# Kernel tuning notes

Measured on AMD Instinct MI355X. Metric: run time of the kernel, lower is better.

## Reference

```python
import jax, jax.numpy as jnp
import numpy as np

EMBED_DIM = 512
NUM_HEADS = 8
HEAD_DIM = EMBED_DIM // NUM_HEADS
SCALE = HEAD_DIM ** -0.5
B, N = 4, 2048


def setup_inputs() -> dict:
    key = jax.random.key(0)
    ks = jax.random.split(key, 6)
    x = jax.random.normal(ks[0], (B, N, EMBED_DIM), dtype=jnp.float32)
    mask = jnp.ones((B, N, N), dtype=jnp.int32)
    # nn.Linear params: weight [out, in], bias [out]
    lim_qkv = 1.0 / np.sqrt(EMBED_DIM)
    qkv_w = jax.random.uniform(ks[1], (3 * EMBED_DIM, EMBED_DIM), jnp.float32, -lim_qkv, lim_qkv)
    qkv_b = jax.random.uniform(ks[2], (3 * EMBED_DIM,), jnp.float32, -lim_qkv, lim_qkv)
    proj_w = jax.random.uniform(ks[3], (EMBED_DIM, EMBED_DIM), jnp.float32, -lim_qkv, lim_qkv)
    proj_b = jax.random.uniform(ks[4], (EMBED_DIM,), jnp.float32, -lim_qkv, lim_qkv)
    return {"x": x, "qkv_w": qkv_w, "qkv_b": qkv_b, "proj_w": proj_w, "proj_b": proj_b, "mask": mask}


def reference(x, qkv_w, qkv_b, proj_w, proj_b, mask):
    Bb, Nn, C = x.shape
    qkv = (jnp.einsum('bnc,oc->bno', x, qkv_w) + qkv_b).reshape(Bb, Nn, 3, NUM_HEADS, HEAD_DIM)
    qkv = jnp.transpose(qkv, (2, 0, 3, 1, 4))
    q, k, v = qkv[0], qkv[1], qkv[2]
    # full score matrix [B,H,N,N] (faithful to the unfused original)
    attn = jnp.einsum('bhnd,bhmd->bhnm', q, k) * SCALE
    attn = jnp.where(mask[:, None, :, :] == 0, -jnp.inf, attn)
    attn = jax.nn.softmax(attn, axis=-1)
    out = jnp.einsum('bhnm,bhmd->bhnd', attn, v)
    out = jnp.transpose(out, (0, 2, 1, 3)).reshape(Bb, Nn, C)
    out = jnp.einsum('bnc,oc->bno', out, proj_w) + proj_b
    return out
```

## Files before the change

### kernel.cpp

```cpp
#include <hip/hip_runtime.h>
#include <hip/hip_bf16.h>
#include <stdint.h>

#define NB 4
#define NH 8
#define SEQ 2048
#define HD 64
#define CDIM 512

using bf16 = __hip_bfloat16;
typedef __attribute__((ext_vector_type(8))) short short8;
typedef __attribute__((ext_vector_type(4))) short short4_t;
typedef __attribute__((ext_vector_type(2))) unsigned int uint2_t;
typedef __attribute__((ext_vector_type(4))) float f32x4;

#define NEG_BIG (-3.0e38f)
#define SOFT_C 0.18033688011112042f

__device__ __forceinline__ short bf16_bits(float x) {
  return __builtin_bit_cast(short, __float2bfloat16(x));
}

__device__ __forceinline__ void pack_p4(float a, float b, float c, float d, short* dst) {
  unsigned lo = (unsigned)(unsigned short)bf16_bits(a) |
                ((unsigned)(unsigned short)bf16_bits(b) << 16);
  unsigned hi = (unsigned)(unsigned short)bf16_bits(c) |
                ((unsigned)(unsigned short)bf16_bits(d) << 16);
  uint2_t t;
  t[0] = lo;
  t[1] = hi;
  *(uint2_t*)dst = t;
}

__device__ __forceinline__ void gld_lds16(const void* g, void* l) {
  __builtin_amdgcn_global_load_lds(
      (const __attribute__((address_space(1))) unsigned int*)g,
      (__attribute__((address_space(3))) unsigned int*)l, 16, 0, 0);
}

#define X4 1048576
#define Q4 196608
#define P4 65536
__global__ __launch_bounds__(256) void prep_cvt(const float* __restrict__ x,
                                                const float* __restrict__ wq,
                                                const float* __restrict__ wp,
                                                short* __restrict__ xb,
                                                short* __restrict__ wqb,
                                                short* __restrict__ wpb) {
  int idx = blockIdx.x * 256 + threadIdx.x;
  int stride = gridDim.x * 256;
  for (int i = idx; i < X4 + Q4 + P4; i += stride) {
    const float* src; short* dst; int off;
    if (i < X4)            { src = x;  dst = xb;  off = i; }
    else if (i < X4 + Q4)  { src = wq; dst = wqb; off = i - X4; }
    else                   { src = wp; dst = wpb; off = i - X4 - Q4; }
    f32x4 v = *(const f32x4*)(src + (size_t)off * 4);
    short4_t o;
    o[0] = bf16_bits(v[0]); o[1] = bf16_bits(v[1]);
    o[2] = bf16_bits(v[2]); o[3] = bf16_bits(v[3]);
    *(short4_t*)(dst + (size_t)off * 4) = o;
  }
}

__global__ __launch_bounds__(256) void qkv_union(const short* __restrict__ Xb,
                                                 const short* __restrict__ Wb,
                                                 const float* __restrict__ bias,
                                                 const int* __restrict__ mask,
                                                 unsigned long long* __restrict__ bits,
                                                 bf16* __restrict__ q,
                                                 bf16* __restrict__ k,
                                                 bf16* __restrict__ vt) {
  __shared__ short Alds[128][32];
  __shared__ short Blds[128][32];
  const int tid = threadIdx.x;
  const int lane = tid & 63;
  const int w = tid >> 6;

  if (blockIdx.x < 512) {
    int wave_g = blockIdx.x * 4 + w;
#pragma unroll 1
    for (int i = 0; i < 32; i++) {
      size_t c = (size_t)i * 2048 + wave_g;
      size_t base = c * 256;
      int v0 = mask[base + 0 * 64 + lane];
      int v1 = mask[base + 1 * 64 + lane];
      int v2 = mask[base + 2 * 64 + lane];
      int v3 = mask[base + 3 * 64 + lane];
      unsigned long long w0 = __ballot(v0 != 0);
      unsigned long long w1 = __ballot(v1 != 0);
      unsigned long long w2 = __ballot(v2 != 0);
      unsigned long long w3 = __ballot(v3 != 0);
      if (lane == 0) {
        bits[c * 4 + 0] = w0; bits[c * 4 + 1] = w1;
        bits[c * 4 + 2] = w2; bits[c * 4 + 3] = w3;
      }
    }
    return;
  }

  const int g = blockIdx.x - 512;
  const int wm = w >> 1, wn = w & 1;
  const int row0 = (g & 63) * 128;
  const int col0 = (g >> 6) * 128;
  const bool isv = (col0 >= 1024);

  f32x4 acc[4][4] = {};
  const int cl = lane & 15;
  const int quad = lane >> 4;

  const int st_r = lane >> 2;
  const int st_gc = (lane & 3) ^ (st_r & 3);
  const int st_col = st_gc * 8;
  const int fc = (quad ^ (cl & 3)) * 8;

  for (int kk = 0; kk < 512; kk += 32) {
#pragma unroll
    for (int t = 0; t < 2; t++) {
      int R = w * 32 + t * 16;
      gld_lds16(&Xb[(size_t)(row0 + R + st_r) * 512 + kk + st_col], &Alds[R][0]);
      gld_lds16(&Wb[(size_t)(col0 + R + st_r) * 512 + kk + st_col], &Blds[R][0]);
    }
    __syncthreads();
    short8 a[4], b[4];
#pragma unroll
    for (int i = 0; i < 4; i++) a[i] = *(const short8*)&Alds[wm * 64 + i * 16 + cl][fc];
#pragma unroll
    for (int j = 0; j < 4; j++) b[j] = *(const short8*)&Blds[wn * 64 + j * 16 + cl][fc];
    if (!isv) {
#pragma unroll
      for (int i = 0; i < 4; i++)
#pragma unroll
        for (int j = 0; j < 4; j++)
          acc[i][j] = __builtin_amdgcn_mfma_f32_16x16x32_bf16(a[i], b[j], acc[i][j], 0, 0, 0);
    } else {
#pragma unroll
      for (int i = 0; i < 4; i++)
#pragma unroll
        for (int j = 0; j < 4; j++)
          acc[i][j] = __builtin_amdgcn_mfma_f32_16x16x32_bf16(b[j], a[i], acc[i][j], 0, 0, 0);
    }
    __syncthreads();
  }

  if (!isv) {
#pragma unroll
    for (int i = 0; i < 4; i++) {
#pragma unroll
      for (int j = 0; j < 4; j++) {
        int col = col0 + wn * 64 + j * 16 + cl;
        float bv = bias[col];
        int which = col >> 9;
        int c = col & 511;
        int h = c >> 6, d = c & 63;
#pragma unroll
        for (int r = 0; r < 4; r++) {
          int row = row0 + wm * 64 + i * 16 + quad * 4 + r;
          int bb = row >> 11, n = row & 2047;
          float val = acc[i][j][r] + bv;
          size_t bh = (size_t)bb * NH + h;
          if (which == 0)      q[(bh * SEQ + n) * HD + d] = __float2bfloat16(val * SOFT_C);
          else                 k[(bh * SEQ + n) * HD + d] = __float2bfloat16(val);
        }
      }
    }
  } else {
#pragma unroll
    for (int i = 0; i < 4; i++) {
#pragma unroll
      for (int j = 0; j < 4; j++) {
        int nrow = row0 + wm * 64 + i * 16 + cl;
        int bb = nrow >> 11, n = nrow & 2047;
#pragma unroll
        for (int r = 0; r < 4; r++) {
          int col = col0 + wn * 64 + j * 16 + quad * 4 + r;
          float bv = bias[col];
          int c = col & 511;
          int h = c >> 6, d = c & 63;
          float val = acc[i][j][r] + bv;
          size_t bh = (size_t)bb * NH + h;
          vt[(bh * HD + d) * SEQ + n] = __float2bfloat16(val);
        }
      }
    }
  }
}

__global__ __launch_bounds__(256) void flash_attn(const bf16* __restrict__ qg,
                                                  const bf16* __restrict__ kg,
                                                  const bf16* __restrict__ vg,
                                                  const unsigned long long* __restrict__ mbits,
                                                  bf16* __restrict__ attn_out) {
  __shared__ short Klds[2][64][64];
  __shared__ short Vlds[2][64][64];
  __shared__ short Plds[4][2][16][72];

  const int tid = threadIdx.x;
  const int lane = tid & 63;
  const int w = tid >> 6;
  const int qt = blockIdx.x;
  const int h = blockIdx.y;
  const int b = blockIdx.z;

  const size_t bh = (size_t)b * NH + h;
  const bf16* qp = qg + bh * SEQ * HD;
  const bf16* kp = kg + bh * SEQ * HD;
  const bf16* vp = vg + bh * HD * SEQ;

  const int cl = lane & 15;
  const int quad = lane >> 4;
  const int koff = quad * 8;
  const int qrow_w = qt * 128 + w * 32;

  const int c0 = ((quad ^ (cl & 7)) * 8);

  const int st_row = lane >> 3;
  const int st_chunk = (lane & 7) ^ st_row;
  const int st_col = st_chunk * 8;

  const unsigned long long* mr0 = mbits + ((size_t)b * SEQ + qt * 128 + w * 32 + cl) * 32;
  const unsigned long long* mr1 = mr0 + 16 * 32;

  short8 aq[2][2];
#pragma unroll
  for (int g = 0; g < 2; g++) {
    aq[g][0] = *(const short8*)&qp[(size_t)(qrow_w + g * 16 + cl) * HD + koff];
    aq[g][1] = *(const short8*)&qp[(size_t)(qrow_w + g * 16 + cl) * HD + 32 + koff];
  }

  short8 ones;
#pragma unroll
  for (int i = 0; i < 8; i++) ones[i] = (short)0x3F80;

  f32x4 o[2][4] = {};
  f32x4 ol[2] = {};

#pragma unroll
  for (int t = 0; t < 2; t++) {
    int rbase = w * 16 + t * 8;
    gld_lds16(&kp[(size_t)(rbase + st_row) * HD + st_col], &Klds[0][rbase][0]);
    gld_lds16(&vp[(size_t)(rbase + st_row) * SEQ + st_col], &Vlds[0][rbase][0]);
  }
  unsigned long long wd_next[2];
  wd_next[0] = mr0[0];
  wd_next[1] = mr1[0];
  __syncthreads();

  for (int kt = 0; kt < 32; kt++) {
    const int cur = kt & 1;

    short8 k0[4], k1[4], vb[2][4];
#pragma unroll
    for (int nb = 0; nb < 4; nb++) {
      k0[nb] = *(const short8*)&Klds[cur][nb * 16 + cl][c0];
      k1[nb] = *(const short8*)&Klds[cur][nb * 16 + cl][c0 ^ 32];
    }
#pragma unroll
    for (int ks = 0; ks < 2; ks++)
#pragma unroll
      for (int db = 0; db < 4; db++)
        vb[ks][db] = *(const short8*)&Vlds[cur][db * 16 + cl][c0 ^ (ks * 32)];

    if (kt + 1 < 32) {
      const int kb2 = (kt + 1) * 64;
#pragma unroll
      for (int t = 0; t < 2; t++) {
        int rbase = w * 16 + t * 8;
        gld_lds16(&kp[(size_t)(kb2 + rbase + st_row) * HD + st_col], &Klds[cur ^ 1][rbase][0]);
        gld_lds16(&vp[(size_t)(rbase + st_row) * SEQ + kb2 + st_col], &Vlds[cur ^ 1][rbase][0]);
      }
    }
    unsigned long long wd[2] = {wd_next[0], wd_next[1]};
    if (kt + 1 < 32) {
      wd_next[0] = mr0[kt + 1];
      wd_next[1] = mr1[kt + 1];
    }

    f32x4 s[2][4];
#pragma unroll
    for (int g = 0; g < 2; g++)
#pragma unroll
      for (int nb = 0; nb < 4; nb++) {
        f32x4 z = {0.f, 0.f, 0.f, 0.f};
        z = __builtin_amdgcn_mfma_f32_16x16x32_bf16(k0[nb], aq[g][0], z, 0, 0, 0);
        s[g][nb] = __builtin_amdgcn_mfma_f32_16x16x32_bf16(k1[nb], aq[g][1], z, 0, 0, 0);
      }

#pragma unroll
    for (int g = 0; g < 2; g++) {
      if (wd[g] != ~0ULL) {
#pragma unroll
        for (int nb = 0; nb < 4; nb++)
#pragma unroll
          for (int r = 0; r < 4; r++)
            if (!((wd[g] >> (nb * 16 + quad * 4 + r)) & 1ULL)) s[g][nb][r] = NEG_BIG;
      }
#pragma unroll
      for (int nb = 0; nb < 4; nb++) {
#pragma unroll
        for (int r = 0; r < 4; r++) s[g][nb][r] = __builtin_amdgcn_exp2f(s[g][nb][r]);
        pack_p4(s[g][nb][0], s[g][nb][1], s[g][nb][2], s[g][nb][3],
                &Plds[w][g][cl][nb * 16 + quad * 4]);
      }
    }

#pragma unroll
    for (int g = 0; g < 2; g++)
#pragma unroll
      for (int ks = 0; ks < 2; ks++) {
        short8 pa = *(const short8*)&Plds[w][g][cl][ks * 32 + koff];
#pragma unroll
        for (int db = 0; db < 4; db++)
          o[g][db] = __builtin_amdgcn_mfma_f32_16x16x32_bf16(pa, vb[ks][db], o[g][db], 0, 0, 0);
        ol[g] = __builtin_amdgcn_mfma_f32_16x16x32_bf16(pa, ones, ol[g], 0, 0, 0);
      }

    __syncthreads();
  }

#pragma unroll
  for (int g = 0; g < 2; g++) {
#pragma unroll
    for (int r = 0; r < 4; r++) {
      float inv = 1.0f / ol[g][r];
      int row = qrow_w + g * 16 + quad * 4 + r;
#pragma unroll
      for (int db = 0; db < 4; db++) {
        float val = o[g][db][r] * inv;
        attn_out[((size_t)b * SEQ + row) * CDIM + h * 64 + db * 16 + cl] = __float2bfloat16(val);
      }
    }
  }
}

__global__ __launch_bounds__(256) void proj_gemm(const bf16* __restrict__ X,
                                                 const short* __restrict__ Wb,
                                                 const float* __restrict__ bias,
                                                 float* __restrict__ out) {
  __shared__ short Alds[128][32];
  __shared__ short Blds[128][32];
  const int tid = threadIdx.x;
  const int lane = tid & 63;
  const int w = tid >> 6;
  const int wm = w >> 1, wn = w & 1;
  const int row0 = blockIdx.x * 128;
  const int col0 = blockIdx.y * 128;

  f32x4 acc[4][4] = {};
  const int cl = lane & 15;
  const int quad = lane >> 4;

  const int st_r = lane >> 2;
  const int st_gc = (lane & 3) ^ (st_r & 3);
  const int st_col = st_gc * 8;
  const int fc = (quad ^ (cl & 3)) * 8;

  for (int kk = 0; kk < 512; kk += 32) {
#pragma unroll
    for (int t = 0; t < 2; t++) {
      int R = w * 32 + t * 16;
      gld_lds16(&X[(size_t)(row0 + R + st_r) * 512 + kk + st_col], &Alds[R][0]);
      gld_lds16(&Wb[(size_t)(col0 + R + st_r) * 512 + kk + st_col], &Blds[R][0]);
    }
    __syncthreads();
    short8 a[4], b[4];
#pragma unroll
    for (int i = 0; i < 4; i++) a[i] = *(const short8*)&Alds[wm * 64 + i * 16 + cl][fc];
#pragma unroll
    for (int j = 0; j < 4; j++) b[j] = *(const short8*)&Blds[wn * 64 + j * 16 + cl][fc];
#pragma unroll
    for (int i = 0; i < 4; i++)
#pragma unroll
      for (int j = 0; j < 4; j++)
        acc[i][j] = __builtin_amdgcn_mfma_f32_16x16x32_bf16(a[i], b[j], acc[i][j], 0, 0, 0);
    __syncthreads();
  }

#pragma unroll
  for (int i = 0; i < 4; i++) {
#pragma unroll
    for (int j = 0; j < 4; j++) {
      int col = col0 + wn * 64 + j * 16 + cl;
      float bv = bias[col];
#pragma unroll
      for (int r = 0; r < 4; r++) {
        int row = row0 + wm * 64 + i * 16 + quad * 4 + r;
        out[(size_t)row * 512 + col] = acc[i][j][r] + bv;
      }
    }
  }
}

extern "C" void kernel_launch(void* const* d_in, const int* in_sizes, int n_in,
                              void* d_out, int out_size, void* d_ws, size_t ws_size,
                              hipStream_t stream) {
  const float* x      = (const float*)d_in[0];
  const float* qkv_w  = (const float*)d_in[1];
  const float* qkv_b  = (const float*)d_in[2];
  const float* proj_w = (const float*)d_in[3];
  const float* proj_b = (const float*)d_in[4];
  const int*   mask   = (const int*)d_in[5];
  float* out = (float*)d_out;

  char* ws = (char*)d_ws;
  bf16* q    = (bf16*)(ws);
  bf16* k    = (bf16*)(ws + 8388608);
  bf16* vt   = (bf16*)(ws + 16777216);
  bf16* attn = (bf16*)(ws + 25165824);
  short* xb  = (short*)(ws + 25165824);
  unsigned long long* mbits = (unsigned long long*)(ws + 33554432);
  short* wqb = (short*)(ws + 35651584);
  short* wpb = (short*)(ws + 37224448);

  prep_cvt<<<dim3(1280), 256, 0, stream>>>(x, qkv_w, proj_w, xb, wqb, wpb);
  qkv_union<<<dim3(512 + 768), 256, 0, stream>>>(xb, wqb, qkv_b, mask, mbits, q, k, vt);
  flash_attn<<<dim3(SEQ / 128, NH, NB), 256, 0, stream>>>(q, k, vt, mbits, attn);
  proj_gemm<<<dim3(64, 4), 256, 0, stream>>>(attn, wpb, proj_b, out);
}
```

Baseline: 222.1 us.

## Split flash attention query tile across 8 waves of 16 rows each

The attention kernel now launches 512 threads per block, with each of 8 waves owning 16 query rows instead of 4 waves owning 32. Per-wave registers for Q fragments, accumulators and scores are halved, and K/V tile loading is spread over more waves. The aim is more latency hiding and occupancy on the attention loop. In exchange, each wave reuses the K/V fragments it reads from LDS over fewer query rows, so LDS read traffic per unit of compute doubles, and block-wide barriers span more waves.

```diff
diff --git a/kernel.cpp b/kernel.cpp
--- a/kernel.cpp
+++ b/kernel.cpp
@@ -185,14 +185,14 @@
   }
 }
 
-__global__ __launch_bounds__(256) void flash_attn(const bf16* __restrict__ qg,
+__global__ __launch_bounds__(512) void flash_attn(const bf16* __restrict__ qg,
                                                   const bf16* __restrict__ kg,
                                                   const bf16* __restrict__ vg,
                                                   const unsigned long long* __restrict__ mbits,
                                                   bf16* __restrict__ attn_out) {
   __shared__ short Klds[2][64][64];
   __shared__ short Vlds[2][64][64];
-  __shared__ short Plds[4][2][16][72];
+  __shared__ short Plds[8][16][72];
 
   const int tid = threadIdx.x;
   const int lane = tid & 63;
@@ -209,7 +209,7 @@
   const int cl = lane & 15;
   const int quad = lane >> 4;
   const int koff = quad * 8;
-  const int qrow_w = qt * 128 + w * 32;
+  const int qrow_w = qt * 128 + w * 16;
 
   const int c0 = ((quad ^ (cl & 7)) * 8);
 
@@ -217,32 +217,24 @@
   const int st_chunk = (lane & 7) ^ st_row;
   const int st_col = st_chunk * 8;
 
-  const unsigned long long* mr0 = mbits + ((size_t)b * SEQ + qt * 128 + w * 32 + cl) * 32;
-  const unsigned long long* mr1 = mr0 + 16 * 32;
-
-  short8 aq[2][2];
-#pragma unroll
-  for (int g = 0; g < 2; g++) {
-    aq[g][0] = *(const short8*)&qp[(size_t)(qrow_w + g * 16 + cl) * HD + koff];
-    aq[g][1] = *(const short8*)&qp[(size_t)(qrow_w + g * 16 + cl) * HD + 32 + koff];
-  }
+  const unsigned long long* mr = mbits + ((size_t)b * SEQ + qt * 128 + w * 16 + cl) * 32;
+
+  short8 aq0 = *(const short8*)&qp[(size_t)(qrow_w + cl) * HD + koff];
+  short8 aq1 = *(const short8*)&qp[(size_t)(qrow_w + cl) * HD + 32 + koff];
 
   short8 ones;
 #pragma unroll
   for (int i = 0; i < 8; i++) ones[i] = (short)0x3F80;
 
-  f32x4 o[2][4] = {};
-  f32x4 ol[2] = {};
-
-#pragma unroll
-  for (int t = 0; t < 2; t++) {
-    int rbase = w * 16 + t * 8;
+  f32x4 o[4] = {};
+  f32x4 ol = {};
+
+  {
+    int rbase = w * 8;
     gld_lds16(&kp[(size_t)(rbase + st_row) * HD + st_col], &Klds[0][rbase][0]);
     gld_lds16(&vp[(size_t)(rbase + st_row) * SEQ + st_col], &Vlds[0][rbase][0]);
   }
-  unsigned long long wd_next[2];
-  wd_next[0] = mr0[0];
-  wd_next[1] = mr1[0];
+  unsigned long long wd_next = mr[0];
   __syncthreads();
 
   for (int kt = 0; kt < 32; kt++) {
@@ -262,72 +254,56 @@
 
     if (kt + 1 < 32) {
       const int kb2 = (kt + 1) * 64;
-#pragma unroll
-      for (int t = 0; t < 2; t++) {
-        int rbase = w * 16 + t * 8;
-        gld_lds16(&kp[(size_t)(kb2 + rbase + st_row) * HD + st_col], &Klds[cur ^ 1][rbase][0]);
-        gld_lds16(&vp[(size_t)(rbase + st_row) * SEQ + kb2 + st_col], &Vlds[cur ^ 1][rbase][0]);
-      }
-    }
-    unsigned long long wd[2] = {wd_next[0], wd_next[1]};
-    if (kt + 1 < 32) {
-      wd_next[0] = mr0[kt + 1];
-      wd_next[1] = mr1[kt + 1];
-    }
-
-    f32x4 s[2][4];
-#pragma unroll
-    for (int g = 0; g < 2; g++)
-#pragma unroll
-      for (int nb = 0; nb < 4; nb++) {
-        f32x4 z = {0.f, 0.f, 0.f, 0.f};
-        z = __builtin_amdgcn_mfma_f32_16x16x32_bf16(k0[nb], aq[g][0], z, 0, 0, 0);
-        s[g][nb] = __builtin_amdgcn_mfma_f32_16x16x32_bf16(k1[nb], aq[g][1], z, 0, 0, 0);
-      }
-
-#pragma unroll
-    for (int g = 0; g < 2; g++) {
-      if (wd[g] != ~0ULL) {
-#pragma unroll
-        for (int nb = 0; nb < 4; nb++)
-#pragma unroll
-          for (int r = 0; r < 4; r++)
-            if (!((wd[g] >> (nb * 16 + quad * 4 + r)) & 1ULL)) s[g][nb][r] = NEG_BIG;
-      }
-#pragma unroll
-      for (int nb = 0; nb < 4; nb++) {
-#pragma unroll
-        for (int r = 0; r < 4; r++) s[g][nb][r] = __builtin_amdgcn_exp2f(s[g][nb][r]);
-        pack_p4(s[g][nb][0], s[g][nb][1], s[g][nb][2], s[g][nb][3],
-                &Plds[w][g][cl][nb * 16 + quad * 4]);
-      }
-    }
-
-#pragma unroll
-    for (int g = 0; g < 2; g++)
-#pragma unroll
-      for (int ks = 0; ks < 2; ks++) {
-        short8 pa = *(const short8*)&Plds[w][g][cl][ks * 32 + koff];
-#pragma unroll
-        for (int db = 0; db < 4; db++)
-          o[g][db] = __builtin_amdgcn_mfma_f32_16x16x32_bf16(pa, vb[ks][db], o[g][db], 0, 0, 0);
-        ol[g] = __builtin_amdgcn_mfma_f32_16x16x32_bf16(pa, ones, ol[g], 0, 0, 0);
-      }
-
-    __syncthreads();
-  }
-
-#pragma unroll
-  for (int g = 0; g < 2; g++) {
-#pragma unroll
-    for (int r = 0; r < 4; r++) {
-      float inv = 1.0f / ol[g][r];
-      int row = qrow_w + g * 16 + quad * 4 + r;
-#pragma unroll
-      for (int db = 0; db < 4; db++) {
-        float val = o[g][db][r] * inv;
-        attn_out[((size_t)b * SEQ + row) * CDIM + h * 64 + db * 16 + cl] = __float2bfloat16(val);
-      }
+      int rbase = w * 8;
+      gld_lds16(&kp[(size_t)(kb2 + rbase + st_row) * HD + st_col], &Klds[cur ^ 1][rbase][0]);
+      gld_lds16(&vp[(size_t)(rbase + st_row) * SEQ + kb2 + st_col], &Vlds[cur ^ 1][rbase][0]);
+    }
+    unsigned long long wd = wd_next;
+    if (kt + 1 < 32) wd_next = mr[kt + 1];
+
+    f32x4 s[4];
+#pragma unroll
+    for (int nb = 0; nb < 4; nb++) {
+      f32x4 z = {0.f, 0.f, 0.f, 0.f};
+      z = __builtin_amdgcn_mfma_f32_16x16x32_bf16(k0[nb], aq0, z, 0, 0, 0);
+      s[nb] = __builtin_amdgcn_mfma_f32_16x16x32_bf16(k1[nb], aq1, z, 0, 0, 0);
+    }
+
+    if (wd != ~0ULL) {
+#pragma unroll
+      for (int nb = 0; nb < 4; nb++)
+#pragma unroll
+        for (int r = 0; r < 4; r++)
+          if (!((wd >> (nb * 16 + quad * 4 + r)) & 1ULL)) s[nb][r] = NEG_BIG;
+    }
+#pragma unroll
+    for (int nb = 0; nb < 4; nb++) {
+#pragma unroll
+      for (int r = 0; r < 4; r++) s[nb][r] = __builtin_amdgcn_exp2f(s[nb][r]);
+      pack_p4(s[nb][0], s[nb][1], s[nb][2], s[nb][3],
+              &Plds[w][cl][nb * 16 + quad * 4]);
+    }
+
+#pragma unroll
+    for (int ks = 0; ks < 2; ks++) {
+      short8 pa = *(const short8*)&Plds[w][cl][ks * 32 + koff];
+#pragma unroll
+      for (int db = 0; db < 4; db++)
+        o[db] = __builtin_amdgcn_mfma_f32_16x16x32_bf16(pa, vb[ks][db], o[db], 0, 0, 0);
+      ol = __builtin_amdgcn_mfma_f32_16x16x32_bf16(pa, ones, ol, 0, 0, 0);
+    }
+
+    __syncthreads();
+  }
+
+#pragma unroll
+  for (int r = 0; r < 4; r++) {
+    float inv = 1.0f / ol[r];
+    int row = qrow_w + quad * 4 + r;
+#pragma unroll
+    for (int db = 0; db < 4; db++) {
+      float val = o[db][r] * inv;
+      attn_out[((size_t)b * SEQ + row) * CDIM + h * 64 + db * 16 + cl] = __float2bfloat16(val);
     }
   }
 }
@@ -413,6 +389,6 @@
 
   prep_cvt<<<dim3(1280), 256, 0, stream>>>(x, qkv_w, proj_w, xb, wqb, wpb);
   qkv_union<<<dim3(512 + 768), 256, 0, stream>>>(xb, wqb, qkv_b, mask, mbits, q, k, vt);
-  flash_attn<<<dim3(SEQ / 128, NH, NB), 256, 0, stream>>>(q, k, vt, mbits, attn);
+  flash_attn<<<dim3(SEQ / 128, NH, NB), 512, 0, stream>>>(q, k, vt, mbits, attn);
   proj_gemm<<<dim3(64, 4), 256, 0, stream>>>(attn, wpb, proj_b, out);
 }
```

After: 224.6 us. About the same (+1.1%).
